# Kernel tuning notes

Hardware: AMD Instinct MI355X
Metric: run time of the kernel (lower is better)

Reference implementation:

```python
import jax, jax.numpy as jnp
import numpy as np

B, N, K = 2, 16384, 16
C_IN, C_OUT, SHARE = 64, 64, 8
ATTN = C_OUT // SHARE  # 8
EPS = 1e-5


def bn(x, gamma, beta):
    # BatchNorm2d_P: normalize over (B, N, K) per channel, training-mode batch stats
    m = jnp.mean(x, axis=(0, 1, 2), keepdims=True)
    v = jnp.var(x, axis=(0, 1, 2), keepdims=True)  # biased variance
    return (x - m) * jax.lax.rsqrt(v + EPS) * gamma + beta


def gather(points, idx):
    # points: (B, N, C), idx: (B, N, K) -> (B, N, K, C)
    b, n, k = idx.shape
    flat = idx.reshape(b, n * k)
    out = jnp.take_along_axis(points, flat[:, :, None], axis=1)
    return out.reshape(b, n, k, points.shape[-1])


def setup_inputs() -> dict:
    key = jax.random.key(0)
    ks = jax.random.split(key, 16)
    w = lambda k_, shp: (jax.random.normal(k_, shp, dtype=jnp.float32) * 0.02)
    inp = {
        "xyz": jax.random.normal(ks[0], (B, N, 3), dtype=jnp.float32),
        "features": jax.random.normal(ks[1], (B, N, C_IN), dtype=jnp.float32),
        "knn_idx": jax.random.randint(ks[2], (B, N, K), 0, N),
        "Wq": w(ks[3], (C_IN, C_OUT)), "bq": jnp.zeros((C_OUT,), jnp.float32),
        "Wk": w(ks[4], (C_IN, C_OUT)), "bk": jnp.zeros((C_OUT,), jnp.float32),
        "Wv": w(ks[5], (C_IN, C_OUT)), "bv": jnp.zeros((C_OUT,), jnp.float32),
        "Wd1": w(ks[6], (3, 3)), "bd1": jnp.zeros((3,), jnp.float32),
        "gamma_d": jnp.ones((3,), jnp.float32), "beta_d": jnp.zeros((3,), jnp.float32),
        "Wd2": w(ks[7], (3, C_OUT)), "bd2": jnp.zeros((C_OUT,), jnp.float32),
        "gamma_g1": jnp.ones((C_OUT,), jnp.float32), "beta_g1": jnp.zeros((C_OUT,), jnp.float32),
        "Wg1": w(ks[8], (C_OUT, ATTN)), "bg1": jnp.zeros((ATTN,), jnp.float32),
        "gamma_g2": jnp.ones((ATTN,), jnp.float32), "beta_g2": jnp.zeros((ATTN,), jnp.float32),
        "Wg2": w(ks[9], (ATTN, ATTN)), "bg2": jnp.zeros((ATTN,), jnp.float32),
    }
    return inp


def reference(xyz, features, knn_idx, Wq, bq, Wk, bk, Wv, bv,
              Wd1, bd1, gamma_d, beta_d, Wd2, bd2,
              gamma_g1, beta_g1, Wg1, bg1, gamma_g2, beta_g2, Wg2, bg2):
    q = features @ Wq + bq                       # (B,N,C_OUT)
    k = gather(features @ Wk + bk, knn_idx)      # (B,N,K,C_OUT)
    v = gather(features @ Wv + bv, knn_idx)      # (B,N,K,C_OUT)
    knn_xyz = gather(xyz, knn_idx)               # (B,N,K,3)
    rel = xyz[:, :, None, :] - knn_xyz           # (B,N,K,3)
    # fc_delta: Linear(3,3) -> BN -> ReLU -> Linear(3,C_OUT)
    pos_enc = jax.nn.relu(bn(rel @ Wd1 + bd1, gamma_d, beta_d)) @ Wd2 + bd2  # (B,N,K,C_OUT)
    # einops.reduce 'b n k (i j) -> b n k j' with j=mid_planes is identity (i=1)
    attn_in = q[:, :, None, :] - k + pos_enc     # (B,N,K,C_OUT)
    # fc_gamma: BN -> ReLU -> Linear(C_OUT,ATTN) -> BN -> ReLU -> Linear(ATTN,ATTN)
    h = jax.nn.relu(bn(attn_in, gamma_g1, beta_g1)) @ Wg1 + bg1  # (B,N,K,ATTN)
    h = jax.nn.relu(bn(h, gamma_g2, beta_g2)) @ Wg2 + bg2        # (B,N,K,ATTN)
    attn = jax.nn.softmax(h, axis=2)             # softmax over K neighbors
    vp = (v + pos_enc).reshape(B, N, K, SHARE, ATTN)
    res = jnp.einsum('bnksa,bnka->bnsa', vp, attn)
    return res.reshape(B, N, C_OUT)
```

## Files before the change

kernel.cpp:

```cpp
#include <hip/hip_runtime.h>
#include <hip/hip_bf16.h>

#define BB 2
#define NN 16384
#define KK 16
#define CC 64
#define AA 8
#define BN_PTS (BB*NN)
#define TOT (BB*NN*KK)
#define EPS 1e-5f

using bf = __hip_bfloat16;

__device__ __forceinline__ float ldf(const float* p, int i) { return p[i]; }
__device__ __forceinline__ float ldf(const bf* p, int i)    { return __bfloat162float(p[i]); }
__device__ __forceinline__ void  stf(float* p, int i, float v) { p[i] = v; }
__device__ __forceinline__ void  stf(bf* p, int i, float v)    { p[i] = __float2bfloat16(v); }

__device__ __forceinline__ float waveReduce(float v) {
    #pragma unroll
    for (int off = 32; off; off >>= 1) v += __shfl_down(v, off, 64);
    return v;
}

__global__ void detect_kernel(const unsigned* __restrict__ gbits, int* __restrict__ flag) {
    if (threadIdx.x == 0 && blockIdx.x == 0)
        *flag = (gbits[0] == 0x3F803F80u) ? 1 : 0;
}

template<typename T, int E>
__global__ __launch_bounds__(192) void qkv_kernel(
    const int* __restrict__ flag,
    const T* __restrict__ feat,
    const T* __restrict__ Wq, const T* __restrict__ bq,
    const T* __restrict__ Wk, const T* __restrict__ bk,
    const T* __restrict__ Wv, const T* __restrict__ bv,
    float* __restrict__ qf, float* __restrict__ kf, float* __restrict__ vf)
{
    if (*flag != E) return;
    __shared__ float fs[32*64];
    const int which = threadIdx.x / 64;
    const int c = threadIdx.x & 63;
    const T* W    = (which == 0) ? Wq : (which == 1) ? Wk : Wv;
    const T* bias = (which == 0) ? bq : (which == 1) ? bk : bv;
    float* out    = (which == 0) ? qf : (which == 1) ? kf : vf;

    float w[64];
    #pragma unroll
    for (int j = 0; j < 64; j++) w[j] = ldf(W, j*64 + c);
    const float bb_ = ldf(bias, c);

    const int row0 = blockIdx.x * 32;
    for (int i = threadIdx.x; i < 32*64; i += 192)
        fs[i] = ldf(feat, row0*64 + i);
    __syncthreads();

    for (int r = 0; r < 32; r++) {
        float acc = bb_;
        #pragma unroll
        for (int j = 0; j < 64; j++) acc = fmaf(fs[r*64 + j], w[j], acc);
        out[(row0 + r)*64 + c] = acc;
    }
}

template<typename T, int E>
__global__ __launch_bounds__(256) void statsd_kernel(
    const int* __restrict__ flag,
    const T* __restrict__ xyz, const int* __restrict__ knn,
    const T* __restrict__ Wd1, const T* __restrict__ bd1,
    float* __restrict__ part,
    float* __restrict__ dx, float* __restrict__ dy, float* __restrict__ dz)
{
    if (*flag != E) return;
    float w[9], bi[3];
    #pragma unroll
    for (int i = 0; i < 9; i++) w[i] = ldf(Wd1, i);
    #pragma unroll
    for (int i = 0; i < 3; i++) bi[i] = ldf(bd1, i);

    float s[6] = {0,0,0,0,0,0};
    const int tid = blockIdx.x * 256 + threadIdx.x;
    for (int p = tid; p < TOT; p += 256*256) {
        const int bn = p >> 4;
        const int b  = bn >> 14;
        const int j  = knn[p];
        const int nb = (b << 14) + j;
        const float r0 = ldf(xyz, bn*3+0) - ldf(xyz, nb*3+0);
        const float r1 = ldf(xyz, bn*3+1) - ldf(xyz, nb*3+1);
        const float r2 = ldf(xyz, bn*3+2) - ldf(xyz, nb*3+2);
        const float d0 = fmaf(r0, w[0], fmaf(r1, w[3], fmaf(r2, w[6], bi[0])));
        const float d1 = fmaf(r0, w[1], fmaf(r1, w[4], fmaf(r2, w[7], bi[1])));
        const float d2 = fmaf(r0, w[2], fmaf(r1, w[5], fmaf(r2, w[8], bi[2])));
        if (dx) { dx[p] = d0; dy[p] = d1; dz[p] = d2; }
        s[0] += d0; s[1] += d1; s[2] += d2;
        s[3] = fmaf(d0, d0, s[3]); s[4] = fmaf(d1, d1, s[4]); s[5] = fmaf(d2, d2, s[5]);
    }
    __shared__ float red[4*6];
    const int lane = threadIdx.x & 63, wave = threadIdx.x >> 6;
    #pragma unroll
    for (int i = 0; i < 6; i++) {
        const float r = waveReduce(s[i]);
        if (lane == 0) red[wave*6 + i] = r;
    }
    __syncthreads();
    if (threadIdx.x < 6)
        part[blockIdx.x*8 + threadIdx.x] =
            red[threadIdx.x] + red[6+threadIdx.x] + red[12+threadIdx.x] + red[18+threadIdx.x];
}

template<typename T, int E>
__global__ void finalize_d(const int* __restrict__ flag,
                           const float* __restrict__ part,
                           const T* __restrict__ gamma, const T* __restrict__ beta,
                           float* __restrict__ coef)
{
    if (*flag != E) return;
    __shared__ float sums[6];
    const int t = threadIdx.x;
    if (t < 6) {
        float s = 0;
        for (int b = 0; b < 256; b++) s += part[b*8 + t];
        sums[t] = s;
    }
    __syncthreads();
    if (t < 3) {
        const float mean = sums[t] / (float)TOT;
        const float var  = sums[3+t] / (float)TOT - mean*mean;
        const float sc   = ldf(gamma, t) * rsqrtf(var + EPS);
        coef[t]   = sc;
        coef[4+t] = ldf(beta, t) - mean*sc;
    }
}

template<typename T, int E>
__global__ __launch_bounds__(256) void statsg1_kernel(
    const int* __restrict__ flag,
    const T* __restrict__ xyz, const int* __restrict__ knn,
    const float* __restrict__ qf, const float* __restrict__ kf,
    const T* __restrict__ Wd1, const T* __restrict__ bd1,
    const T* __restrict__ Wd2, const T* __restrict__ bd2,
    const float* __restrict__ coefd, float* __restrict__ part,
    const float* __restrict__ dx, const float* __restrict__ dy,
    const float* __restrict__ dz, bf* __restrict__ aibuf)
{
    if (*flag != E) return;
    const int lane = threadIdx.x & 63, wave = threadIdx.x >> 6;
    float w1[9], b1[3], sc[3], sh[3];
    #pragma unroll
    for (int i = 0; i < 9; i++) w1[i] = ldf(Wd1, i);
    #pragma unroll
    for (int i = 0; i < 3; i++) { b1[i] = ldf(bd1, i); sc[i] = coefd[i]; sh[i] = coefd[4+i]; }
    const float w2a = ldf(Wd2, lane), w2b = ldf(Wd2, 64+lane), w2c = ldf(Wd2, 128+lane);
    const float bd2c = ldf(bd2, lane);

    float sum = 0.f, sq = 0.f;
    for (int bn = blockIdx.x*4 + wave; bn < BN_PTS; bn += 2048*4) {
        const int b = bn >> 14;
        const float qv = qf[bn*64 + lane];
        float x0 = 0.f, x1 = 0.f, x2 = 0.f;
        if (!dx) { x0 = ldf(xyz, bn*3+0); x1 = ldf(xyz, bn*3+1); x2 = ldf(xyz, bn*3+2); }
        #pragma unroll
        for (int k = 0; k < 16; k++) {
            const int it = bn*16 + k;
            const int j  = knn[it];
            const int nb = (b << 14) + j;
            float d0, d1, d2;
            if (dx) {
                d0 = dx[it]; d1 = dy[it]; d2 = dz[it];
            } else {
                const float r0 = x0 - ldf(xyz, nb*3+0);
                const float r1 = x1 - ldf(xyz, nb*3+1);
                const float r2 = x2 - ldf(xyz, nb*3+2);
                d0 = fmaf(r0, w1[0], fmaf(r1, w1[3], fmaf(r2, w1[6], b1[0])));
                d1 = fmaf(r0, w1[1], fmaf(r1, w1[4], fmaf(r2, w1[7], b1[1])));
                d2 = fmaf(r0, w1[2], fmaf(r1, w1[5], fmaf(r2, w1[8], b1[2])));
            }
            d0 = fmaxf(fmaf(d0, sc[0], sh[0]), 0.f);
            d1 = fmaxf(fmaf(d1, sc[1], sh[1]), 0.f);
            d2 = fmaxf(fmaf(d2, sc[2], sh[2]), 0.f);
            const float pos = fmaf(d0, w2a, fmaf(d1, w2b, fmaf(d2, w2c, bd2c)));
            const float at = qv - kf[nb*64 + lane] + pos;
            if (aibuf) aibuf[(size_t)it*64 + lane] = __float2bfloat16(at);
            sum += at; sq = fmaf(at, at, sq);
        }
    }
    __shared__ float ls[4][64], lq[4][64];
    ls[wave][lane] = sum; lq[wave][lane] = sq;
    __syncthreads();
    if (threadIdx.x < 64) {
        float a = 0.f, q = 0.f;
        #pragma unroll
        for (int w = 0; w < 4; w++) { a += ls[w][lane]; q += lq[w][lane]; }
        part[blockIdx.x*128 + lane]      = a;
        part[blockIdx.x*128 + 64 + lane] = q;
    }
}

template<int E>
__global__ __launch_bounds__(256) void reduce_g1(const int* __restrict__ flag,
                           const float* __restrict__ part, float* __restrict__ partB)
{
    if (*flag != E) return;
    __shared__ float red[2][128];
    const int t = threadIdx.x;
    const int col = t & 127, chunk = t >> 7;
    const int r0 = blockIdx.x * 32;
    float s = 0.f;
    #pragma unroll
    for (int j = 0; j < 16; j++) s += part[(r0 + chunk + 2*j)*128 + col];
    red[chunk][col] = s;
    __syncthreads();
    if (t < 128) partB[blockIdx.x*128 + t] = red[0][t] + red[1][t];
}

template<typename T, int E>
__global__ __launch_bounds__(512) void finalize_g1(const int* __restrict__ flag,
                            const float* __restrict__ partB,
                            const T* __restrict__ gamma, const T* __restrict__ beta,
                            float* __restrict__ coef)
{
    if (*flag != E) return;
    __shared__ float red[4][128];
    __shared__ float sums[128];
    const int t = threadIdx.x;
    const int col = t & 127, chunk = t >> 7;
    float s = 0.f;
    #pragma unroll
    for (int j = 0; j < 16; j++) s += partB[(chunk + 4*j)*128 + col];
    red[chunk][col] = s;
    __syncthreads();
    if (t < 128) sums[t] = red[0][t] + red[1][t] + red[2][t] + red[3][t];
    __syncthreads();
    if (t < 64) {
        const float mean = sums[t] / (float)TOT;
        const float var  = sums[64+t] / (float)TOT - mean*mean;
        const float sc   = ldf(gamma, t) * rsqrtf(var + EPS);
        coef[t]    = sc;
        coef[64+t] = ldf(beta, t) - mean*sc;
    }
}

template<typename T, int E>
__global__ __launch_bounds__(256) void h1_fast(
    const int* __restrict__ flag,
    const unsigned* __restrict__ aibuf,
    const float* __restrict__ coefg1,
    const T* __restrict__ Wg1, const T* __restrict__ bg1,
    float* __restrict__ h1, float* __restrict__ part)
{
    if (*flag != E) return;
    __shared__ float wg1s[512];
    __shared__ float scs[64], shs[64];
    __shared__ float ssum[4][8], ssq[4][8];
    const int t = threadIdx.x, lane = t & 63, wave = t >> 6;
    for (int i = t; i < 512; i += 256) wg1s[i] = ldf(Wg1, i);
    if (t < 64) { scs[t] = coefg1[t]; shs[t] = coefg1[64 + t]; }
    __syncthreads();

    const size_t item = (size_t)blockIdx.x*256 + t;
    const uint4* src = (const uint4*)aibuf + item*8;
    float h[8];
    #pragma unroll
    for (int a = 0; a < 8; a++) h[a] = ldf(bg1, a);
    #pragma unroll
    for (int cb = 0; cb < 8; cb++) {
        const uint4 u = src[cb];
        const unsigned uu[4] = {u.x, u.y, u.z, u.w};
        #pragma unroll
        for (int q = 0; q < 4; q++) {
            const int c0 = cb*8 + q*2;
            const float xlo = __uint_as_float(uu[q] << 16);
            const float xhi = __uint_as_float(uu[q] & 0xffff0000u);
            const float g0 = fmaxf(fmaf(xlo, scs[c0],   shs[c0]),   0.f);
            const float g1 = fmaxf(fmaf(xhi, scs[c0+1], shs[c0+1]), 0.f);
            #pragma unroll
            for (int a = 0; a < 8; a++) {
                h[a] = fmaf(g0, wg1s[c0*8 + a], h[a]);
                h[a] = fmaf(g1, wg1s[(c0+1)*8 + a], h[a]);
            }
        }
    }
    float4* hp = (float4*)(h1 + item*8);
    hp[0] = make_float4(h[0], h[1], h[2], h[3]);
    hp[1] = make_float4(h[4], h[5], h[6], h[7]);

    #pragma unroll
    for (int a = 0; a < 8; a++) {
        const float rs = waveReduce(h[a]);
        const float rq = waveReduce(h[a]*h[a]);
        if (lane == 0) { ssum[wave][a] = rs; ssq[wave][a] = rq; }
    }
    __syncthreads();
    if (t < 8) {
        part[blockIdx.x*16 + t]     = ssum[0][t] + ssum[1][t] + ssum[2][t] + ssum[3][t];
        part[blockIdx.x*16 + 8 + t] = ssq[0][t]  + ssq[1][t]  + ssq[2][t]  + ssq[3][t];
    }
}

#define H1_PAD 68
template<typename T, int E>
__global__ __launch_bounds__(256, 4) void h1_kernel(
    const int* __restrict__ flag,
    const T* __restrict__ xyz, const int* __restrict__ knn,
    const float* __restrict__ qf, const float* __restrict__ kf,
    const T* __restrict__ Wd1, const T* __restrict__ bd1,
    const T* __restrict__ Wd2, const T* __restrict__ bd2,
    const float* __restrict__ coefd, const float* __restrict__ coefg1,
    const T* __restrict__ Wg1, const T* __restrict__ bg1,
    float* __restrict__ h1, float* __restrict__ part)
{
    if (*flag != E) return;
    __shared__ float xs[128*H1_PAD];
    __shared__ float wg1s[512];
    __shared__ float ssum[4][8], ssq[4][8];
    const int t = threadIdx.x;
    const int lane = t & 63, wave = t >> 6;

    for (int i = t; i < 512; i += 256) wg1s[i] = ldf(Wg1, i);

    float w1[9], b1[3], scd[3], shd[3];
    #pragma unroll
    for (int i = 0; i < 9; i++) w1[i] = ldf(Wd1, i);
    #pragma unroll
    for (int i = 0; i < 3; i++) { b1[i] = ldf(bd1, i); scd[i] = coefd[i]; shd[i] = coefd[4+i]; }
    const float w2a = ldf(Wd2, lane), w2b = ldf(Wd2, 64+lane), w2c = ldf(Wd2, 128+lane);
    const float bd2c = ldf(bd2, lane);
    const float sc1 = coefg1[lane], sh1 = coefg1[64+lane];
    const int lslot = (lane < 32) ? lane : lane + 4;

    #pragma unroll
    for (int g = 0; g < 2; g++) {
        const int pl = wave*2 + g;
        const int bn = blockIdx.x*8 + pl;
        const int b  = bn >> 14;
        const float qv = qf[bn*64 + lane];
        const float x0 = ldf(xyz, bn*3+0), x1 = ldf(xyz, bn*3+1), x2 = ldf(xyz, bn*3+2);
        #pragma unroll
        for (int k = 0; k < 16; k++) {
            const int j  = knn[bn*16 + k];
            const int nb = (b << 14) + j;
            const float r0 = x0 - ldf(xyz, nb*3+0);
            const float r1 = x1 - ldf(xyz, nb*3+1);
            const float r2 = x2 - ldf(xyz, nb*3+2);
            float d0 = fmaf(r0, w1[0], fmaf(r1, w1[3], fmaf(r2, w1[6], b1[0])));
            float d1 = fmaf(r0, w1[1], fmaf(r1, w1[4], fmaf(r2, w1[7], b1[1])));
            float d2 = fmaf(r0, w1[2], fmaf(r1, w1[5], fmaf(r2, w1[8], b1[2])));
            d0 = fmaxf(fmaf(d0, scd[0], shd[0]), 0.f);
            d1 = fmaxf(fmaf(d1, scd[1], shd[1]), 0.f);
            d2 = fmaxf(fmaf(d2, scd[2], shd[2]), 0.f);
            const float pos = fmaf(d0, w2a, fmaf(d1, w2b, fmaf(d2, w2c, bd2c)));
            const float at = qv - kf[nb*64 + lane] + pos;
            xs[(pl*16 + k)*H1_PAD + lslot] = fmaxf(fmaf(at, sc1, sh1), 0.f);
        }
    }
    __syncthreads();

    const int item = t >> 1;
    const int half = t & 1;
    float h[8];
    #pragma unroll
    for (int a = 0; a < 8; a++) h[a] = half ? 0.f : ldf(bg1, a);
    const float4* xr = (const float4*)(xs + item*H1_PAD + half*36);
    const float* wbase = wg1s + half*256;
    #pragma unroll
    for (int cb = 0; cb < 8; cb++) {
        const float4 xv = xr[cb];
        #pragma unroll
        for (int jj = 0; jj < 4; jj++) {
            const float x = (jj == 0) ? xv.x : (jj == 1) ? xv.y : (jj == 2) ? xv.z : xv.w;
            const float4 wa = *(const float4*)&wbase[(cb*4 + jj)*8];
            const float4 wb = *(const float4*)&wbase[(cb*4 + jj)*8 + 4];
            h[0] = fmaf(x, wa.x, h[0]); h[1] = fmaf(x, wa.y, h[1]);
            h[2] = fmaf(x, wa.z, h[2]); h[3] = fmaf(x, wa.w, h[3]);
            h[4] = fmaf(x, wb.x, h[4]); h[5] = fmaf(x, wb.y, h[5]);
            h[6] = fmaf(x, wb.z, h[6]); h[7] = fmaf(x, wb.w, h[7]);
        }
    }
    #pragma unroll
    for (int a = 0; a < 8; a++) h[a] += __shfl_xor(h[a], 1, 64);

    const int it = blockIdx.x*128 + item;
    if (half == 0) {
        float4* hp = (float4*)(h1 + (size_t)it*8);
        hp[0] = make_float4(h[0], h[1], h[2], h[3]);
        hp[1] = make_float4(h[4], h[5], h[6], h[7]);
    }

    #pragma unroll
    for (int a = 0; a < 8; a++) {
        const float rs = waveReduce(h[a]);
        const float rq = waveReduce(h[a]*h[a]);
        if (lane == 0) { ssum[wave][a] = 0.5f*rs; ssq[wave][a] = 0.5f*rq; }
    }
    __syncthreads();
    if (t < 8) {
        part[blockIdx.x*16 + t]     = ssum[0][t] + ssum[1][t] + ssum[2][t] + ssum[3][t];
        part[blockIdx.x*16 + 8 + t] = ssq[0][t]  + ssq[1][t]  + ssq[2][t]  + ssq[3][t];
    }
}

template<int E>
__global__ __launch_bounds__(256) void reduce_g2(const int* __restrict__ flag,
                           const float* __restrict__ part, float* __restrict__ partB,
                           int rows)
{
    if (*flag != E) return;
    __shared__ float red[16][16];
    const int t = threadIdx.x;
    const int col = t & 15, chunk = t >> 4;
    const int rpb = rows >> 6;
    const int r0 = blockIdx.x * rpb;
    float s = 0.f;
    for (int r = chunk; r < rpb; r += 16) s += part[(r0 + r)*16 + col];
    red[chunk][col] = s;
    __syncthreads();
    if (t < 16) {
        float a = 0.f;
        #pragma unroll
        for (int c = 0; c < 16; c++) a += red[c][t];
        partB[blockIdx.x*16 + t] = a;
    }
}

template<typename T, int E>
__global__ __launch_bounds__(256) void finalize_g2(const int* __restrict__ flag,
                            const float* __restrict__ partB,
                            const T* __restrict__ gamma, const T* __restrict__ beta,
                            float* __restrict__ coef)
{
    if (*flag != E) return;
    __shared__ float red[16][16];
    __shared__ float sums[16];
    const int t = threadIdx.x;
    const int col = t & 15, chunk = t >> 4;
    float s = 0.f;
    #pragma unroll
    for (int j = 0; j < 4; j++) s += partB[(chunk + 16*j)*16 + col];
    red[chunk][col] = s;
    __syncthreads();
    if (t < 16) {
        float a = 0.f;
        #pragma unroll
        for (int c = 0; c < 16; c++) a += red[c][t];
        sums[t] = a;
    }
    __syncthreads();
    if (t < 8) {
        const float mean = sums[t] / (float)TOT;
        const float var  = sums[8+t] / (float)TOT - mean*mean;
        const float sc   = ldf(gamma, t) * rsqrtf(var + EPS);
        coef[t]   = sc;
        coef[8+t] = ldf(beta, t) - mean*sc;
    }
}

template<typename T, int E>
__global__ __launch_bounds__(256) void out_kernel(
    const int* __restrict__ flag,
    const T* __restrict__ xyz, const int* __restrict__ knn,
    const float* __restrict__ vf, const float* __restrict__ h1,
    const T* __restrict__ Wd1, const T* __restrict__ bd1,
    const T* __restrict__ Wd2, const T* __restrict__ bd2,
    const float* __restrict__ coefd, const float* __restrict__ coefg2,
    const T* __restrict__ Wg2, const T* __restrict__ bg2,
    const float* __restrict__ dx, const float* __restrict__ dy,
    const float* __restrict__ dz,
    T* __restrict__ out)
{
    if (*flag != E) return;
    __shared__ float g[4][128];
    __shared__ float hh[4][128];
    __shared__ float dd[4][16][3];
    __shared__ int   idxs[4][16];
    __shared__ float wg2[64];
    const int t = threadIdx.x;
    const int bn0 = blockIdx.x * 4;

    if (t < 64) wg2[t] = ldf(Wg2, t);

    {
        const int p = t >> 6, f = t & 63;
        const int base = (bn0 + p) * 128;
        #pragma unroll
        for (int i = 0; i < 2; i++) {
            const int ff = f + i*64;
            const int a = ff & 7;
            const float v = h1[base + ff];
            g[p][ff] = fmaxf(fmaf(v, coefg2[a], coefg2[8 + a]), 0.f);
        }
    }
    if (t < 64) {
        const int p = t >> 4, k = t & 15;
        const int bn = bn0 + p;
        const int b = bn >> 14;
        const int it = bn*16 + k;
        const int j = knn[it];
        idxs[p][k] = j;
        float d0, d1, d2;
        if (dx) {
            d0 = dx[it]; d1 = dy[it]; d2 = dz[it];
        } else {
            const int nb = (b << 14) + j;
            const float r0 = ldf(xyz, bn*3+0) - ldf(xyz, nb*3+0);
            const float r1 = ldf(xyz, bn*3+1) - ldf(xyz, nb*3+1);
            const float r2 = ldf(xyz, bn*3+2) - ldf(xyz, nb*3+2);
            d0 = fmaf(r0, ldf(Wd1,0), fmaf(r1, ldf(Wd1,3), fmaf(r2, ldf(Wd1,6), ldf(bd1,0))));
            d1 = fmaf(r0, ldf(Wd1,1), fmaf(r1, ldf(Wd1,4), fmaf(r2, ldf(Wd1,7), ldf(bd1,1))));
            d2 = fmaf(r0, ldf(Wd1,2), fmaf(r1, ldf(Wd1,5), fmaf(r2, ldf(Wd1,8), ldf(bd1,2))));
        }
        dd[p][k][0] = fmaxf(fmaf(d0, coefd[0], coefd[4]), 0.f);
        dd[p][k][1] = fmaxf(fmaf(d1, coefd[1], coefd[5]), 0.f);
        dd[p][k][2] = fmaxf(fmaf(d2, coefd[2], coefd[6]), 0.f);
    }
    __syncthreads();

    {
        #pragma unroll
        for (int i = 0; i < 2; i++) {
            const int o = t + i*256;
            const int p = o >> 7, f = o & 127;
            const int a = f & 7, k = f >> 3;
            float acc = ldf(bg2, a);
            #pragma unroll
            for (int jj = 0; jj < 8; jj++) acc = fmaf(g[p][k*8 + jj], wg2[jj*8 + a], acc);
            hh[p][f] = acc;
        }
    }
    __syncthreads();

    if (t < 32) {
        const int p = t >> 3, a = t & 7;
        float m = -1e30f;
        #pragma unroll
        for (int k = 0; k < 16; k++) m = fmaxf(m, hh[p][k*8 + a]);
        float e[16]; float s = 0.f;
        #pragma unroll
        for (int k = 0; k < 16; k++) { e[k] = __expf(hh[p][k*8 + a] - m); s += e[k]; }
        const float inv = 1.f / s;
        #pragma unroll
        for (int k = 0; k < 16; k++) hh[p][k*8 + a] = e[k] * inv;
    }
    __syncthreads();

    {
        const int p = t >> 6, c = t & 63, a = c & 7;
        const int bn = bn0 + p;
        const int b = bn >> 14;
        const float w0 = ldf(Wd2, c), w1 = ldf(Wd2, 64 + c), w2 = ldf(Wd2, 128 + c);
        const float bd2c = ldf(bd2, c);
        float acc = 0.f;
        #pragma unroll
        for (int k = 0; k < 16; k++) {
            const int j = idxs[p][k];
            const float pos = fmaf(dd[p][k][0], w0, fmaf(dd[p][k][1], w1, fmaf(dd[p][k][2], w2, bd2c)));
            const float vv = vf[((b << 14) + j)*64 + c] + pos;
            acc = fmaf(vv, hh[p][k*8 + a], acc);
        }
        stf(out, bn*64 + c, acc);
    }
}

#define WS_BIG_FLOATS 29108384ull

template<typename T, int E>
static void launch_all(void* const* d_in, void* d_out, float* ws, const int* flag,
                       bool big, hipStream_t stream) {
    const T*   xyz   = (const T*) d_in[0];
    const T*   feat  = (const T*) d_in[1];
    const int* knn   = (const int*)d_in[2];
    const T*   Wq    = (const T*) d_in[3];
    const T*   bq    = (const T*) d_in[4];
    const T*   Wk    = (const T*) d_in[5];
    const T*   bk    = (const T*) d_in[6];
    const T*   Wv    = (const T*) d_in[7];
    const T*   bv    = (const T*) d_in[8];
    const T*   Wd1   = (const T*) d_in[9];
    const T*   bd1   = (const T*) d_in[10];
    const T*   gd    = (const T*) d_in[11];
    const T*   betad = (const T*) d_in[12];
    const T*   Wd2   = (const T*) d_in[13];
    const T*   bd2   = (const T*) d_in[14];
    const T*   gg1   = (const T*) d_in[15];
    const T*   bg1b  = (const T*) d_in[16];
    const T*   Wg1   = (const T*) d_in[17];
    const T*   bg1   = (const T*) d_in[18];
    const T*   gg2   = (const T*) d_in[19];
    const T*   bg2b  = (const T*) d_in[20];
    const T*   Wg2   = (const T*) d_in[21];
    const T*   bg2   = (const T*) d_in[22];
    T* out = (T*)d_out;

    float* qf      = ws;
    float* kf      = ws + 2097152;
    float* vf      = ws + 4194304;
    float* h1      = ws + 6291456;
    float* part_d  = ws + 10485760;
    float* partA   = ws + 10487808;
    float* partB   = ws + 10749952;
    float* coef_d  = ws + 10758144;
    float* coef_g1 = ws + 10758152;
    float* coef_g2 = ws + 10758280;
    float* dx      = big ? ws + 10758304 : nullptr;
    float* dy      = big ? ws + 11282592 : nullptr;
    float* dz      = big ? ws + 11806880 : nullptr;
    bf*    aibuf   = big ? (bf*)(ws + 12331168) : nullptr;

    qkv_kernel<T,E><<<1024, 192, 0, stream>>>(flag, feat, Wq, bq, Wk, bk, Wv, bv, qf, kf, vf);
    statsd_kernel<T,E><<<256, 256, 0, stream>>>(flag, xyz, knn, Wd1, bd1, part_d, dx, dy, dz);
    finalize_d<T,E><<<1, 64, 0, stream>>>(flag, part_d, gd, betad, coef_d);
    statsg1_kernel<T,E><<<2048, 256, 0, stream>>>(flag, xyz, knn, qf, kf, Wd1, bd1, Wd2, bd2,
                                                  coef_d, partA, dx, dy, dz, aibuf);
    reduce_g1<E><<<64, 256, 0, stream>>>(flag, partA, partB);
    finalize_g1<T,E><<<1, 512, 0, stream>>>(flag, partB, gg1, bg1b, coef_g1);
    if (big) {
        h1_fast<T,E><<<2048, 256, 0, stream>>>(flag, (const unsigned*)aibuf, coef_g1,
                                               Wg1, bg1, h1, partA);
        reduce_g2<E><<<64, 256, 0, stream>>>(flag, partA, partB, 2048);
    } else {
        h1_kernel<T,E><<<4096, 256, 0, stream>>>(flag, xyz, knn, qf, kf, Wd1, bd1, Wd2, bd2,
                                                 coef_d, coef_g1, Wg1, bg1, h1, partA);
        reduce_g2<E><<<64, 256, 0, stream>>>(flag, partA, partB, 4096);
    }
    finalize_g2<T,E><<<1, 256, 0, stream>>>(flag, partB, gg2, bg2b, coef_g2);
    out_kernel<T,E><<<8192, 256, 0, stream>>>(flag, xyz, knn, vf, h1, Wd1, bd1, Wd2, bd2,
                                              coef_d, coef_g2, Wg2, bg2, dx, dy, dz, out);
}

extern "C" void kernel_launch(void* const* d_in, const int* in_sizes, int n_in,
                              void* d_out, int out_size, void* d_ws, size_t ws_size,
                              hipStream_t stream) {
    float* ws = (float*)d_ws;
    int* flag = (int*)(ws + 10758296);
    const bool big = ws_size >= WS_BIG_FLOATS * 4ull;

    detect_kernel<<<1, 1, 0, stream>>>((const unsigned*)d_in[11], flag);

    launch_all<float, 0>(d_in, d_out, ws, flag, big, stream);
    launch_all<bf,    1>(d_in, d_out, ws, flag, big, stream);
}
```

Before: 277.6 us.

## Merge dtype-specialized launches into single kernels and store K projection in bf16

Each stage used to be launched twice, once per input dtype, with the inactive copy returning early on a device flag. Now each kernel is launched once and branches on the flag inside the kernel to a templated body, using dynamic shared memory. This roughly halves the number of kernel launches. The K projection buffer is also stored in bf16, which halves the bytes moved by the random neighbor gather in statsg1 (and in h1_kernel on the fallback path). The trade-off is extra rounding error in k.

After: 270.7 us. 2.5% less time.

```diff
diff --git a/kernel.cpp b/kernel.cpp
--- a/kernel.cpp
+++ b/kernel.cpp
@@ -1,5 +1,6 @@
 #include <hip/hip_runtime.h>
 #include <hip/hip_bf16.h>
+#include <type_traits>
 
 #define BB 2
 #define NN 16384
@@ -12,10 +13,16 @@
 
 using bf = __hip_bfloat16;
 
-__device__ __forceinline__ float ldf(const float* p, int i) { return p[i]; }
-__device__ __forceinline__ float ldf(const bf* p, int i)    { return __bfloat162float(p[i]); }
-__device__ __forceinline__ void  stf(float* p, int i, float v) { p[i] = v; }
-__device__ __forceinline__ void  stf(bf* p, int i, float v)    { p[i] = __float2bfloat16(v); }
+__device__ __forceinline__ float b2f(bf x) { return __bfloat162float(x); }
+
+template<typename T> __device__ __forceinline__ float ldt(const void* p, int i) {
+    if constexpr (std::is_same<T, bf>::value) return b2f(((const bf*)p)[i]);
+    else return ((const float*)p)[i];
+}
+template<typename T> __device__ __forceinline__ void stt(void* p, int i, float v) {
+    if constexpr (std::is_same<T, bf>::value) ((bf*)p)[i] = __float2bfloat16(v);
+    else ((float*)p)[i] = v;
+}
 
 __device__ __forceinline__ float waveReduce(float v) {
     #pragma unroll
@@ -28,55 +35,57 @@
         *flag = (gbits[0] == 0x3F803F80u) ? 1 : 0;
 }
 
-template<typename T, int E>
+template<typename T>
+__device__ void qkv_body(float* smem,
+    const void* feat, const void* Wq, const void* bq, const void* Wk, const void* bk,
+    const void* Wv, const void* bv, float* qf, bf* kfb, float* vf)
+{
+    float* fs = smem;
+    const int which = threadIdx.x / 64;
+    const int c = threadIdx.x & 63;
+    const void* W    = (which == 0) ? Wq : (which == 1) ? Wk : Wv;
+    const void* bias = (which == 0) ? bq : (which == 1) ? bk : bv;
+
+    float w[64];
+    #pragma unroll
+    for (int j = 0; j < 64; j++) w[j] = ldt<T>(W, j*64 + c);
+    const float bb_ = ldt<T>(bias, c);
+
+    const int row0 = blockIdx.x * 32;
+    for (int i = threadIdx.x; i < 32*64; i += 192)
+        fs[i] = ldt<T>(feat, row0*64 + i);
+    __syncthreads();
+
+    for (int r = 0; r < 32; r++) {
+        float acc = bb_;
+        #pragma unroll
+        for (int j = 0; j < 64; j++) acc = fmaf(fs[r*64 + j], w[j], acc);
+        const int idx = (row0 + r)*64 + c;
+        if (which == 1)      kfb[idx] = __float2bfloat16(acc);
+        else if (which == 0) qf[idx] = acc;
+        else                 vf[idx] = acc;
+    }
+}
 __global__ __launch_bounds__(192) void qkv_kernel(
     const int* __restrict__ flag,
-    const T* __restrict__ feat,
-    const T* __restrict__ Wq, const T* __restrict__ bq,
-    const T* __restrict__ Wk, const T* __restrict__ bk,
-    const T* __restrict__ Wv, const T* __restrict__ bv,
-    float* __restrict__ qf, float* __restrict__ kf, float* __restrict__ vf)
-{
-    if (*flag != E) return;
-    __shared__ float fs[32*64];
-    const int which = threadIdx.x / 64;
-    const int c = threadIdx.x & 63;
-    const T* W    = (which == 0) ? Wq : (which == 1) ? Wk : Wv;
-    const T* bias = (which == 0) ? bq : (which == 1) ? bk : bv;
-    float* out    = (which == 0) ? qf : (which == 1) ? kf : vf;
-
-    float w[64];
-    #pragma unroll
-    for (int j = 0; j < 64; j++) w[j] = ldf(W, j*64 + c);
-    const float bb_ = ldf(bias, c);
-
-    const int row0 = blockIdx.x * 32;
-    for (int i = threadIdx.x; i < 32*64; i += 192)
-        fs[i] = ldf(feat, row0*64 + i);
-    __syncthreads();
-
-    for (int r = 0; r < 32; r++) {
-        float acc = bb_;
-        #pragma unroll
-        for (int j = 0; j < 64; j++) acc = fmaf(fs[r*64 + j], w[j], acc);
-        out[(row0 + r)*64 + c] = acc;
-    }
-}
-
-template<typename T, int E>
-__global__ __launch_bounds__(256) void statsd_kernel(
-    const int* __restrict__ flag,
-    const T* __restrict__ xyz, const int* __restrict__ knn,
-    const T* __restrict__ Wd1, const T* __restrict__ bd1,
-    float* __restrict__ part,
-    float* __restrict__ dx, float* __restrict__ dy, float* __restrict__ dz)
-{
-    if (*flag != E) return;
+    const void* feat, const void* Wq, const void* bq, const void* Wk, const void* bk,
+    const void* Wv, const void* bv, float* qf, bf* kfb, float* vf)
+{
+    extern __shared__ float smem[];
+    if (*flag) qkv_body<bf>(smem, feat, Wq, bq, Wk, bk, Wv, bv, qf, kfb, vf);
+    else       qkv_body<float>(smem, feat, Wq, bq, Wk, bk, Wv, bv, qf, kfb, vf);
+}
+
+template<typename T>
+__device__ void statsd_body(float* smem,
+    const void* xyz, const int* knn, const void* Wd1, const void* bd1,
+    float* part, float* dx, float* dy, float* dz)
+{
     float w[9], bi[3];
     #pragma unroll
-    for (int i = 0; i < 9; i++) w[i] = ldf(Wd1, i);
-    #pragma unroll
-    for (int i = 0; i < 3; i++) bi[i] = ldf(bd1, i);
+    for (int i = 0; i < 9; i++) w[i] = ldt<T>(Wd1, i);
+    #pragma unroll
+    for (int i = 0; i < 3; i++) bi[i] = ldt<T>(bd1, i);
 
     float s[6] = {0,0,0,0,0,0};
     const int tid = blockIdx.x * 256 + threadIdx.x;
@@ -85,9 +94,9 @@
         const int b  = bn >> 14;
         const int j  = knn[p];
         const int nb = (b << 14) + j;
-        const float r0 = ldf(xyz, bn*3+0) - ldf(xyz, nb*3+0);
-        const float r1 = ldf(xyz, bn*3+1) - ldf(xyz, nb*3+1);
-        const float r2 = ldf(xyz, bn*3+2) - ldf(xyz, nb*3+2);
+        const float r0 = ldt<T>(xyz, bn*3+0) - ldt<T>(xyz, nb*3+0);
+        const float r1 = ldt<T>(xyz, bn*3+1) - ldt<T>(xyz, nb*3+1);
+        const float r2 = ldt<T>(xyz, bn*3+2) - ldt<T>(xyz, nb*3+2);
         const float d0 = fmaf(r0, w[0], fmaf(r1, w[3], fmaf(r2, w[6], bi[0])));
         const float d1 = fmaf(r0, w[1], fmaf(r1, w[4], fmaf(r2, w[7], bi[1])));
         const float d2 = fmaf(r0, w[2], fmaf(r1, w[5], fmaf(r2, w[8], bi[2])));
@@ -95,7 +104,7 @@
         s[0] += d0; s[1] += d1; s[2] += d2;
         s[3] = fmaf(d0, d0, s[3]); s[4] = fmaf(d1, d1, s[4]); s[5] = fmaf(d2, d2, s[5]);
     }
-    __shared__ float red[4*6];
+    float* red = smem;
     const int lane = threadIdx.x & 63, wave = threadIdx.x >> 6;
     #pragma unroll
     for (int i = 0; i < 6; i++) {
@@ -107,15 +116,20 @@
         part[blockIdx.x*8 + threadIdx.x] =
             red[threadIdx.x] + red[6+threadIdx.x] + red[12+threadIdx.x] + red[18+threadIdx.x];
 }
-
-template<typename T, int E>
-__global__ void finalize_d(const int* __restrict__ flag,
-                           const float* __restrict__ part,
-                           const T* __restrict__ gamma, const T* __restrict__ beta,
-                           float* __restrict__ coef)
-{
-    if (*flag != E) return;
-    __shared__ float sums[6];
+__global__ __launch_bounds__(256) void statsd_kernel(
+    const int* __restrict__ flag,
+    const void* xyz, const int* __restrict__ knn, const void* Wd1, const void* bd1,
+    float* part, float* dx, float* dy, float* dz)
+{
+    extern __shared__ float smem[];
+    if (*flag) statsd_body<bf>(smem, xyz, knn, Wd1, bd1, part, dx, dy, dz);
+    else       statsd_body<float>(smem, xyz, knn, Wd1, bd1, part, dx, dy, dz);
+}
+
+template<typename T>
+__device__ void finalize_d_body(float* sums,
+    const float* part, const void* gamma, const void* beta, float* coef)
+{
     const int t = threadIdx.x;
     if (t < 6) {
         float s = 0;
@@ -126,39 +140,41 @@
     if (t < 3) {
         const float mean = sums[t] / (float)TOT;
         const float var  = sums[3+t] / (float)TOT - mean*mean;
-        const float sc   = ldf(gamma, t) * rsqrtf(var + EPS);
+        const float sc   = ldt<T>(gamma, t) * rsqrtf(var + EPS);
         coef[t]   = sc;
-        coef[4+t] = ldf(beta, t) - mean*sc;
-    }
-}
-
-template<typename T, int E>
-__global__ __launch_bounds__(256) void statsg1_kernel(
-    const int* __restrict__ flag,
-    const T* __restrict__ xyz, const int* __restrict__ knn,
-    const float* __restrict__ qf, const float* __restrict__ kf,
-    const T* __restrict__ Wd1, const T* __restrict__ bd1,
-    const T* __restrict__ Wd2, const T* __restrict__ bd2,
-    const float* __restrict__ coefd, float* __restrict__ part,
-    const float* __restrict__ dx, const float* __restrict__ dy,
-    const float* __restrict__ dz, bf* __restrict__ aibuf)
-{
-    if (*flag != E) return;
+        coef[4+t] = ldt<T>(beta, t) - mean*sc;
+    }
+}
+__global__ void finalize_d(const int* __restrict__ flag, const float* __restrict__ part,
+                           const void* gamma, const void* beta, float* coef)
+{
+    extern __shared__ float smem[];
+    if (*flag) finalize_d_body<bf>(smem, part, gamma, beta, coef);
+    else       finalize_d_body<float>(smem, part, gamma, beta, coef);
+}
+
+template<typename T>
+__device__ void statsg1_body(float* smem,
+    const void* xyz, const int* knn, const float* qf, const bf* kfb,
+    const void* Wd1, const void* bd1, const void* Wd2, const void* bd2,
+    const float* coefd, float* part,
+    const float* dx, const float* dy, const float* dz, bf* aibuf)
+{
     const int lane = threadIdx.x & 63, wave = threadIdx.x >> 6;
     float w1[9], b1[3], sc[3], sh[3];
     #pragma unroll
-    for (int i = 0; i < 9; i++) w1[i] = ldf(Wd1, i);
-    #pragma unroll
-    for (int i = 0; i < 3; i++) { b1[i] = ldf(bd1, i); sc[i] = coefd[i]; sh[i] = coefd[4+i]; }
-    const float w2a = ldf(Wd2, lane), w2b = ldf(Wd2, 64+lane), w2c = ldf(Wd2, 128+lane);
-    const float bd2c = ldf(bd2, lane);
+    for (int i = 0; i < 9; i++) w1[i] = ldt<T>(Wd1, i);
+    #pragma unroll
+    for (int i = 0; i < 3; i++) { b1[i] = ldt<T>(bd1, i); sc[i] = coefd[i]; sh[i] = coefd[4+i]; }
+    const float w2a = ldt<T>(Wd2, lane), w2b = ldt<T>(Wd2, 64+lane), w2c = ldt<T>(Wd2, 128+lane);
+    const float bd2c = ldt<T>(bd2, lane);
 
     float sum = 0.f, sq = 0.f;
     for (int bn = blockIdx.x*4 + wave; bn < BN_PTS; bn += 2048*4) {
         const int b = bn >> 14;
         const float qv = qf[bn*64 + lane];
         float x0 = 0.f, x1 = 0.f, x2 = 0.f;
-        if (!dx) { x0 = ldf(xyz, bn*3+0); x1 = ldf(xyz, bn*3+1); x2 = ldf(xyz, bn*3+2); }
+        if (!dx) { x0 = ldt<T>(xyz, bn*3+0); x1 = ldt<T>(xyz, bn*3+1); x2 = ldt<T>(xyz, bn*3+2); }
         #pragma unroll
         for (int k = 0; k < 16; k++) {
             const int it = bn*16 + k;
@@ -168,9 +184,9 @@
             if (dx) {
                 d0 = dx[it]; d1 = dy[it]; d2 = dz[it];
             } else {
-                const float r0 = x0 - ldf(xyz, nb*3+0);
-                const float r1 = x1 - ldf(xyz, nb*3+1);
-                const float r2 = x2 - ldf(xyz, nb*3+2);
+                const float r0 = x0 - ldt<T>(xyz, nb*3+0);
+                const float r1 = x1 - ldt<T>(xyz, nb*3+1);
+                const float r2 = x2 - ldt<T>(xyz, nb*3+2);
                 d0 = fmaf(r0, w1[0], fmaf(r1, w1[3], fmaf(r2, w1[6], b1[0])));
                 d1 = fmaf(r0, w1[1], fmaf(r1, w1[4], fmaf(r2, w1[7], b1[1])));
                 d2 = fmaf(r0, w1[2], fmaf(r1, w1[5], fmaf(r2, w1[8], b1[2])));
@@ -179,28 +195,39 @@
             d1 = fmaxf(fmaf(d1, sc[1], sh[1]), 0.f);
             d2 = fmaxf(fmaf(d2, sc[2], sh[2]), 0.f);
             const float pos = fmaf(d0, w2a, fmaf(d1, w2b, fmaf(d2, w2c, bd2c)));
-            const float at = qv - kf[nb*64 + lane] + pos;
+            const float at = qv - b2f(kfb[nb*64 + lane]) + pos;
             if (aibuf) aibuf[(size_t)it*64 + lane] = __float2bfloat16(at);
             sum += at; sq = fmaf(at, at, sq);
         }
     }
-    __shared__ float ls[4][64], lq[4][64];
-    ls[wave][lane] = sum; lq[wave][lane] = sq;
+    float* ls = smem;
+    float* lq = smem + 256;
+    ls[wave*64 + lane] = sum; lq[wave*64 + lane] = sq;
     __syncthreads();
     if (threadIdx.x < 64) {
         float a = 0.f, q = 0.f;
         #pragma unroll
-        for (int w = 0; w < 4; w++) { a += ls[w][lane]; q += lq[w][lane]; }
+        for (int w = 0; w < 4; w++) { a += ls[w*64 + lane]; q += lq[w*64 + lane]; }
         part[blockIdx.x*128 + lane]      = a;
         part[blockIdx.x*128 + 64 + lane] = q;
     }
 }
-
-template<int E>
-__global__ __launch_bounds__(256) void reduce_g1(const int* __restrict__ flag,
-                           const float* __restrict__ part, float* __restrict__ partB)
-{
-    if (*flag != E) return;
+__global__ __launch_bounds__(256) void statsg1_kernel(
+    const int* __restrict__ flag,
+    const void* xyz, const int* __restrict__ knn, const float* __restrict__ qf,
+    const bf* __restrict__ kfb,
+    const void* Wd1, const void* bd1, const void* Wd2, const void* bd2,
+    const float* __restrict__ coefd, float* part,
+    const float* dx, const float* dy, const float* dz, bf* aibuf)
+{
+    extern __shared__ float smem[];
+    if (*flag) statsg1_body<bf>(smem, xyz, knn, qf, kfb, Wd1, bd1, Wd2, bd2, coefd, part, dx, dy, dz, aibuf);
+    else       statsg1_body<float>(smem, xyz, knn, qf, kfb, Wd1, bd1, Wd2, bd2, coefd, part, dx, dy, dz, aibuf);
+}
+
+__global__ __launch_bounds__(256) void reduce_g1(const float* __restrict__ part,
+                                                 float* __restrict__ partB)
+{
     __shared__ float red[2][128];
     const int t = threadIdx.x;
     const int col = t & 127, chunk = t >> 7;
@@ -213,47 +240,49 @@
     if (t < 128) partB[blockIdx.x*128 + t] = red[0][t] + red[1][t];
 }
 
-template<typename T, int E>
-__global__ __launch_bounds__(512) void finalize_g1(const int* __restrict__ flag,
-                            const float* __restrict__ partB,
-                            const T* __restrict__ gamma, const T* __restrict__ beta,
-                            float* __restrict__ coef)
-{
-    if (*flag != E) return;
-    __shared__ float red[4][128];
-    __shared__ float sums[128];
+template<typename T>
+__device__ void finalize_g1_body(float* smem,
+    const float* partB, const void* gamma, const void* beta, float* coef)
+{
+    float* red  = smem;
+    float* sums = smem + 512;
     const int t = threadIdx.x;
     const int col = t & 127, chunk = t >> 7;
     float s = 0.f;
     #pragma unroll
     for (int j = 0; j < 16; j++) s += partB[(chunk + 4*j)*128 + col];
-    red[chunk][col] = s;
-    __syncthreads();
-    if (t < 128) sums[t] = red[0][t] + red[1][t] + red[2][t] + red[3][t];
+    red[chunk*128 + col] = s;
+    __syncthreads();
+    if (t < 128) sums[t] = red[t] + red[128+t] + red[256+t] + red[384+t];
     __syncthreads();
     if (t < 64) {
         const float mean = sums[t] / (float)TOT;
         const float var  = sums[64+t] / (float)TOT - mean*mean;
-        const float sc   = ldf(gamma, t) * rsqrtf(var + EPS);
+        const float sc   = ldt<T>(gamma, t) * rsqrtf(var + EPS);
         coef[t]    = sc;
-        coef[64+t] = ldf(beta, t) - mean*sc;
-    }
-}
-
-template<typename T, int E>
-__global__ __launch_bounds__(256) void h1_fast(
-    const int* __restrict__ flag,
-    const unsigned* __restrict__ aibuf,
-    const float* __restrict__ coefg1,
-    const T* __restrict__ Wg1, const T* __restrict__ bg1,
-    float* __restrict__ h1, float* __restrict__ part)
-{
-    if (*flag != E) return;
-    __shared__ float wg1s[512];
-    __shared__ float scs[64], shs[64];
-    __shared__ float ssum[4][8], ssq[4][8];
+        coef[64+t] = ldt<T>(beta, t) - mean*sc;
+    }
+}
+__global__ __launch_bounds__(512) void finalize_g1(const int* __restrict__ flag,
+    const float* __restrict__ partB, const void* gamma, const void* beta, float* coef)
+{
+    extern __shared__ float smem[];
+    if (*flag) finalize_g1_body<bf>(smem, partB, gamma, beta, coef);
+    else       finalize_g1_body<float>(smem, partB, gamma, beta, coef);
+}
+
+template<typename T>
+__device__ void h1_fast_body(float* smem,
+    const unsigned* aibuf, const float* coefg1, const void* Wg1, const void* bg1,
+    float* h1, float* part)
+{
+    float* wg1s = smem;
+    float* scs  = smem + 512;
+    float* shs  = smem + 576;
+    float* ssum = smem + 640;
+    float* ssq  = smem + 672;
     const int t = threadIdx.x, lane = t & 63, wave = t >> 6;
-    for (int i = t; i < 512; i += 256) wg1s[i] = ldf(Wg1, i);
+    for (int i = t; i < 512; i += 256) wg1s[i] = ldt<T>(Wg1, i);
     if (t < 64) { scs[t] = coefg1[t]; shs[t] = coefg1[64 + t]; }
     __syncthreads();
 
@@ -261,7 +290,7 @@
     const uint4* src = (const uint4*)aibuf + item*8;
     float h[8];
     #pragma unroll
-    for (int a = 0; a < 8; a++) h[a] = ldf(bg1, a);
+    for (int a = 0; a < 8; a++) h[a] = ldt<T>(bg1, a);
     #pragma unroll
     for (int cb = 0; cb < 8; cb++) {
         const uint4 u = src[cb];
@@ -288,43 +317,47 @@
     for (int a = 0; a < 8; a++) {
         const float rs = waveReduce(h[a]);
         const float rq = waveReduce(h[a]*h[a]);
-        if (lane == 0) { ssum[wave][a] = rs; ssq[wave][a] = rq; }
+        if (lane == 0) { ssum[wave*8 + a] = rs; ssq[wave*8 + a] = rq; }
     }
     __syncthreads();
     if (t < 8) {
-        part[blockIdx.x*16 + t]     = ssum[0][t] + ssum[1][t] + ssum[2][t] + ssum[3][t];
-        part[blockIdx.x*16 + 8 + t] = ssq[0][t]  + ssq[1][t]  + ssq[2][t]  + ssq[3][t];
-    }
+        part[blockIdx.x*16 + t]     = ssum[t] + ssum[8+t] + ssum[16+t] + ssum[24+t];
+        part[blockIdx.x*16 + 8 + t] = ssq[t]  + ssq[8+t]  + ssq[16+t]  + ssq[24+t];
+    }
+}
+__global__ __launch_bounds__(256) void h1_fast(const int* __restrict__ flag,
+    const unsigned* __restrict__ aibuf, const float* __restrict__ coefg1,
+    const void* Wg1, const void* bg1, float* h1, float* part)
+{
+    extern __shared__ float smem[];
+    if (*flag) h1_fast_body<bf>(smem, aibuf, coefg1, Wg1, bg1, h1, part);
+    else       h1_fast_body<float>(smem, aibuf, coefg1, Wg1, bg1, h1, part);
 }
 
 #define H1_PAD 68
-template<typename T, int E>
-__global__ __launch_bounds__(256, 4) void h1_kernel(
-    const int* __restrict__ flag,
-    const T* __restrict__ xyz, const int* __restrict__ knn,
-    const float* __restrict__ qf, const float* __restrict__ kf,
-    const T* __restrict__ Wd1, const T* __restrict__ bd1,
-    const T* __restrict__ Wd2, const T* __restrict__ bd2,
-    const float* __restrict__ coefd, const float* __restrict__ coefg1,
-    const T* __restrict__ Wg1, const T* __restrict__ bg1,
-    float* __restrict__ h1, float* __restrict__ part)
-{
-    if (*flag != E) return;
-    __shared__ float xs[128*H1_PAD];
-    __shared__ float wg1s[512];
-    __shared__ float ssum[4][8], ssq[4][8];
+template<typename T>
+__device__ void h1_body(float* smem,
+    const void* xyz, const int* knn, const float* qf, const bf* kfb,
+    const void* Wd1, const void* bd1, const void* Wd2, const void* bd2,
+    const float* coefd, const float* coefg1, const void* Wg1, const void* bg1,
+    float* h1, float* part)
+{
+    float* xs   = smem;
+    float* wg1s = smem + 8704;
+    float* ssum = smem + 9216;
+    float* ssq  = smem + 9248;
     const int t = threadIdx.x;
     const int lane = t & 63, wave = t >> 6;
 
-    for (int i = t; i < 512; i += 256) wg1s[i] = ldf(Wg1, i);
+    for (int i = t; i < 512; i += 256) wg1s[i] = ldt<T>(Wg1, i);
 
     float w1[9], b1[3], scd[3], shd[3];
     #pragma unroll
-    for (int i = 0; i < 9; i++) w1[i] = ldf(Wd1, i);
-    #pragma unroll
-    for (int i = 0; i < 3; i++) { b1[i] = ldf(bd1, i); scd[i] = coefd[i]; shd[i] = coefd[4+i]; }
-    const float w2a = ldf(Wd2, lane), w2b = ldf(Wd2, 64+lane), w2c = ldf(Wd2, 128+lane);
-    const float bd2c = ldf(bd2, lane);
+    for (int i = 0; i < 9; i++) w1[i] = ldt<T>(Wd1, i);
+    #pragma unroll
+    for (int i = 0; i < 3; i++) { b1[i] = ldt<T>(bd1, i); scd[i] = coefd[i]; shd[i] = coefd[4+i]; }
+    const float w2a = ldt<T>(Wd2, lane), w2b = ldt<T>(Wd2, 64+lane), w2c = ldt<T>(Wd2, 128+lane);
+    const float bd2c = ldt<T>(bd2, lane);
     const float sc1 = coefg1[lane], sh1 = coefg1[64+lane];
     const int lslot = (lane < 32) ? lane : lane + 4;
 
@@ -334,14 +367,14 @@
         const int bn = blockIdx.x*8 + pl;
         const int b  = bn >> 14;
         const float qv = qf[bn*64 + lane];
-        const float x0 = ldf(xyz, bn*3+0), x1 = ldf(xyz, bn*3+1), x2 = ldf(xyz, bn*3+2);
+        const float x0 = ldt<T>(xyz, bn*3+0), x1 = ldt<T>(xyz, bn*3+1), x2 = ldt<T>(xyz, bn*3+2);
         #pragma unroll
         for (int k = 0; k < 16; k++) {
             const int j  = knn[bn*16 + k];
             const int nb = (b << 14) + j;
-            const float r0 = x0 - ldf(xyz, nb*3+0);
-            const float r1 = x1 - ldf(xyz, nb*3+1);
-            const float r2 = x2 - ldf(xyz, nb*3+2);
+            const float r0 = x0 - ldt<T>(xyz, nb*3+0);
+            const float r1 = x1 - ldt<T>(xyz, nb*3+1);
+            const float r2 = x2 - ldt<T>(xyz, nb*3+2);
             float d0 = fmaf(r0, w1[0], fmaf(r1, w1[3], fmaf(r2, w1[6], b1[0])));
             float d1 = fmaf(r0, w1[1], fmaf(r1, w1[4], fmaf(r2, w1[7], b1[1])));
             float d2 = fmaf(r0, w1[2], fmaf(r1, w1[5], fmaf(r2, w1[8], b1[2])));
@@ -349,7 +382,7 @@
             d1 = fmaxf(fmaf(d1, scd[1], shd[1]), 0.f);
             d2 = fmaxf(fmaf(d2, scd[2], shd[2]), 0.f);
             const float pos = fmaf(d0, w2a, fmaf(d1, w2b, fmaf(d2, w2c, bd2c)));
-            const float at = qv - kf[nb*64 + lane] + pos;
+            const float at = qv - b2f(kfb[nb*64 + lane]) + pos;
             xs[(pl*16 + k)*H1_PAD + lslot] = fmaxf(fmaf(at, sc1, sh1), 0.f);
         }
     }
@@ -359,7 +392,7 @@
     const int half = t & 1;
     float h[8];
     #pragma unroll
-    for (int a = 0; a < 8; a++) h[a] = half ? 0.f : ldf(bg1, a);
+    for (int a = 0; a < 8; a++) h[a] = half ? 0.f : ldt<T>(bg1, a);
     const float4* xr = (const float4*)(xs + item*H1_PAD + half*36);
     const float* wbase = wg1s + half*256;
     #pragma unroll
@@ -385,26 +418,33 @@
         hp[0] = make_float4(h[0], h[1], h[2], h[3]);
         hp[1] = make_float4(h[4], h[5], h[6], h[7]);
     }
-
     #pragma unroll
     for (int a = 0; a < 8; a++) {
         const float rs = waveReduce(h[a]);
         const float rq = waveReduce(h[a]*h[a]);
-        if (lane == 0) { ssum[wave][a] = 0.5f*rs; ssq[wave][a] = 0.5f*rq; }
+        if (lane == 0) { ssum[wave*8 + a] = 0.5f*rs; ssq[wave*8 + a] = 0.5f*rq; }
     }
     __syncthreads();
     if (t < 8) {
-        part[blockIdx.x*16 + t]     = ssum[0][t] + ssum[1][t] + ssum[2][t] + ssum[3][t];
-        part[blockIdx.x*16 + 8 + t] = ssq[0][t]  + ssq[1][t]  + ssq[2][t]  + ssq[3][t];
-    }
-}
-
-template<int E>
-__global__ __launch_bounds__(256) void reduce_g2(const int* __restrict__ flag,
-                           const float* __restrict__ part, float* __restrict__ partB,
-                           int rows)
-{
-    if (*flag != E) return;
+        part[blockIdx.x*16 + t]     = ssum[t] + ssum[8+t] + ssum[16+t] + ssum[24+t];
+        part[blockIdx.x*16 + 8 + t] = ssq[t]  + ssq[8+t]  + ssq[16+t]  + ssq[24+t];
+    }
+}
+__global__ __launch_bounds__(256, 4) void h1_kernel(const int* __restrict__ flag,
+    const void* xyz, const int* __restrict__ knn, const float* __restrict__ qf,
+    const bf* __restrict__ kfb,
+    const void* Wd1, const void* bd1, const void* Wd2, const void* bd2,
+    const float* __restrict__ coefd, const float* __restrict__ coefg1,
+    const void* Wg1, const void* bg1, float* h1, float* part)
+{
+    extern __shared__ float smem[];
+    if (*flag) h1_body<bf>(smem, xyz, knn, qf, kfb, Wd1, bd1, Wd2, bd2, coefd, coefg1, Wg1, bg1, h1, part);
+    else       h1_body<float>(smem, xyz, knn, qf, kfb, Wd1, bd1, Wd2, bd2, coefd, coefg1, Wg1, bg1, h1, part);
+}
+
+__global__ __launch_bounds__(256) void reduce_g2(const float* __restrict__ part,
+                                                 float* __restrict__ partB, int rows)
+{
     __shared__ float red[16][16];
     const int t = threadIdx.x;
     const int col = t & 15, chunk = t >> 4;
@@ -422,61 +462,58 @@
     }
 }
 
-template<typename T, int E>
-__global__ __launch_bounds__(256) void finalize_g2(const int* __restrict__ flag,
-                            const float* __restrict__ partB,
-                            const T* __restrict__ gamma, const T* __restrict__ beta,
-                            float* __restrict__ coef)
-{
-    if (*flag != E) return;
-    __shared__ float red[16][16];
-    __shared__ float sums[16];
+template<typename T>
+__device__ void finalize_g2_body(float* smem,
+    const float* partB, const void* gamma, const void* beta, float* coef)
+{
+    float* red  = smem;
+    float* sums = smem + 256;
     const int t = threadIdx.x;
     const int col = t & 15, chunk = t >> 4;
     float s = 0.f;
     #pragma unroll
     for (int j = 0; j < 4; j++) s += partB[(chunk + 16*j)*16 + col];
-    red[chunk][col] = s;
+    red[chunk*16 + col] = s;
     __syncthreads();
     if (t < 16) {
         float a = 0.f;
         #pragma unroll
-        for (int c = 0; c < 16; c++) a += red[c][t];
+        for (int c = 0; c < 16; c++) a += red[c*16 + t];
         sums[t] = a;
     }
     __syncthreads();
     if (t < 8) {
         const float mean = sums[t] / (float)TOT;
         const float var  = sums[8+t] / (float)TOT - mean*mean;
-        const float sc   = ldf(gamma, t) * rsqrtf(var + EPS);
+        const float sc   = ldt<T>(gamma, t) * rsqrtf(var + EPS);
         coef[t]   = sc;
-        coef[8+t] = ldf(beta, t) - mean*sc;
-    }
-}
-
-template<typename T, int E>
-__global__ __launch_bounds__(256) void out_kernel(
-    const int* __restrict__ flag,
-    const T* __restrict__ xyz, const int* __restrict__ knn,
-    const float* __restrict__ vf, const float* __restrict__ h1,
-    const T* __restrict__ Wd1, const T* __restrict__ bd1,
-    const T* __restrict__ Wd2, const T* __restrict__ bd2,
-    const float* __restrict__ coefd, const float* __restrict__ coefg2,
-    const T* __restrict__ Wg2, const T* __restrict__ bg2,
-    const float* __restrict__ dx, const float* __restrict__ dy,
-    const float* __restrict__ dz,
-    T* __restrict__ out)
-{
-    if (*flag != E) return;
-    __shared__ float g[4][128];
-    __shared__ float hh[4][128];
-    __shared__ float dd[4][16][3];
-    __shared__ int   idxs[4][16];
-    __shared__ float wg2[64];
+        coef[8+t] = ldt<T>(beta, t) - mean*sc;
+    }
+}
+__global__ __launch_bounds__(256) void finalize_g2(const int* __restrict__ flag,
+    const float* __restrict__ partB, const void* gamma, const void* beta, float* coef)
+{
+    extern __shared__ float smem[];
+    if (*flag) finalize_g2_body<bf>(smem, partB, gamma, beta, coef);
+    else       finalize_g2_body<float>(smem, partB, gamma, beta, coef);
+}
+
+template<typename T>
+__device__ void out_body(float* smem,
+    const void* xyz, const int* knn, const float* vf, const float* h1,
+    const void* Wd1, const void* bd1, const void* Wd2, const void* bd2,
+    const float* coefd, const float* coefg2, const void* Wg2, const void* bg2,
+    const float* dx, const float* dy, const float* dz, void* out)
+{
+    float* g   = smem;
+    float* hh  = smem + 512;
+    float* dd  = smem + 1024;
+    float* wg2 = smem + 1216;
+    int*  idxs = (int*)(smem + 1280);
     const int t = threadIdx.x;
     const int bn0 = blockIdx.x * 4;
 
-    if (t < 64) wg2[t] = ldf(Wg2, t);
+    if (t < 64) wg2[t] = ldt<T>(Wg2, t);
 
     {
         const int p = t >> 6, f = t & 63;
@@ -486,7 +523,7 @@
             const int ff = f + i*64;
             const int a = ff & 7;
             const float v = h1[base + ff];
-            g[p][ff] = fmaxf(fmaf(v, coefg2[a], coefg2[8 + a]), 0.f);
+            g[p*128 + ff] = fmaxf(fmaf(v, coefg2[a], coefg2[8 + a]), 0.f);
         }
     }
     if (t < 64) {
@@ -495,22 +532,22 @@
         const int b = bn >> 14;
         const int it = bn*16 + k;
         const int j = knn[it];
-        idxs[p][k] = j;
+        idxs[p*16 + k] = j;
         float d0, d1, d2;
         if (dx) {
             d0 = dx[it]; d1 = dy[it]; d2 = dz[it];
         } else {
             const int nb = (b << 14) + j;
-            const float r0 = ldf(xyz, bn*3+0) - ldf(xyz, nb*3+0);
-            const float r1 = ldf(xyz, bn*3+1) - ldf(xyz, nb*3+1);
-            const float r2 = ldf(xyz, bn*3+2) - ldf(xyz, nb*3+2);
-            d0 = fmaf(r0, ldf(Wd1,0), fmaf(r1, ldf(Wd1,3), fmaf(r2, ldf(Wd1,6), ldf(bd1,0))));
-            d1 = fmaf(r0, ldf(Wd1,1), fmaf(r1, ldf(Wd1,4), fmaf(r2, ldf(Wd1,7), ldf(bd1,1))));
-            d2 = fmaf(r0, ldf(Wd1,2), fmaf(r1, ldf(Wd1,5), fmaf(r2, ldf(Wd1,8), ldf(bd1,2))));
-        }
-        dd[p][k][0] = fmaxf(fmaf(d0, coefd[0], coefd[4]), 0.f);
-        dd[p][k][1] = fmaxf(fmaf(d1, coefd[1], coefd[5]), 0.f);
-        dd[p][k][2] = fmaxf(fmaf(d2, coefd[2], coefd[6]), 0.f);
+            const float r0 = ldt<T>(xyz, bn*3+0) - ldt<T>(xyz, nb*3+0);
+            const float r1 = ldt<T>(xyz, bn*3+1) - ldt<T>(xyz, nb*3+1);
+            const float r2 = ldt<T>(xyz, bn*3+2) - ldt<T>(xyz, nb*3+2);
+            d0 = fmaf(r0, ldt<T>(Wd1,0), fmaf(r1, ldt<T>(Wd1,3), fmaf(r2, ldt<T>(Wd1,6), ldt<T>(bd1,0))));
+            d1 = fmaf(r0, ldt<T>(Wd1,1), fmaf(r1, ldt<T>(Wd1,4), fmaf(r2, ldt<T>(Wd1,7), ldt<T>(bd1,1))));
+            d2 = fmaf(r0, ldt<T>(Wd1,2), fmaf(r1, ldt<T>(Wd1,5), fmaf(r2, ldt<T>(Wd1,8), ldt<T>(bd1,2))));
+        }
+        dd[(p*16 + k)*3 + 0] = fmaxf(fmaf(d0, coefd[0], coefd[4]), 0.f);
+        dd[(p*16 + k)*3 + 1] = fmaxf(fmaf(d1, coefd[1], coefd[5]), 0.f);
+        dd[(p*16 + k)*3 + 2] = fmaxf(fmaf(d2, coefd[2], coefd[6]), 0.f);
     }
     __syncthreads();
 
@@ -520,10 +557,10 @@
             const int o = t + i*256;
             const int p = o >> 7, f = o & 127;
             const int a = f & 7, k = f >> 3;
-            float acc = ldf(bg2, a);
+            float acc = ldt<T>(bg2, a);
             #pragma unroll
-            for (int jj = 0; jj < 8; jj++) acc = fmaf(g[p][k*8 + jj], wg2[jj*8 + a], acc);
-            hh[p][f] = acc;
+            for (int jj = 0; jj < 8; jj++) acc = fmaf(g[p*128 + k*8 + jj], wg2[jj*8 + a], acc);
+            hh[p*128 + f] = acc;
         }
     }
     __syncthreads();
@@ -532,13 +569,13 @@
         const int p = t >> 3, a = t & 7;
         float m = -1e30f;
         #pragma unroll
-        for (int k = 0; k < 16; k++) m = fmaxf(m, hh[p][k*8 + a]);
+        for (int k = 0; k < 16; k++) m = fmaxf(m, hh[p*128 + k*8 + a]);
         float e[16]; float s = 0.f;
         #pragma unroll
-        for (int k = 0; k < 16; k++) { e[k] = __expf(hh[p][k*8 + a] - m); s += e[k]; }
+        for (int k = 0; k < 16; k++) { e[k] = __expf(hh[p*128 + k*8 + a] - m); s += e[k]; }
         const float inv = 1.f / s;
         #pragma unroll
-        for (int k = 0; k < 16; k++) hh[p][k*8 + a] = e[k] * inv;
+        for (int k = 0; k < 16; k++) hh[p*128 + k*8 + a] = e[k] * inv;
     }
     __syncthreads();
 
@@ -546,95 +583,83 @@
         const int p = t >> 6, c = t & 63, a = c & 7;
         const int bn = bn0 + p;
         const int b = bn >> 14;
-        const float w0 = ldf(Wd2, c), w1 = ldf(Wd2, 64 + c), w2 = ldf(Wd2, 128 + c);
-        const float bd2c = ldf(bd2, c);
+        const float w0 = ldt<T>(Wd2, c), w1 = ldt<T>(Wd2, 64 + c), w2 = ldt<T>(Wd2, 128 + c);
+        const float bd2c = ldt<T>(bd2, c);
         float acc = 0.f;
         #pragma unroll
         for (int k = 0; k < 16; k++) {
-            const int j = idxs[p][k];
-            const float pos = fmaf(dd[p][k][0], w0, fmaf(dd[p][k][1], w1, fmaf(dd[p][k][2], w2, bd2c)));
+            const int j = idxs[p*16 + k];
+            const float pos = fmaf(dd[(p*16+k)*3+0], w0, fmaf(dd[(p*16+k)*3+1], w1,
+                              fmaf(dd[(p*16+k)*3+2], w2, bd2c)));
             const float vv = vf[((b << 14) + j)*64 + c] + pos;
-            acc = fmaf(vv, hh[p][k*8 + a], acc);
-        }
-        stf(out, bn*64 + c, acc);
-    }
-}
-
-#define WS_BIG_FLOATS 29108384ull
-
-template<typename T, int E>
-static void launch_all(void* const* d_in, void* d_out, float* ws, const int* flag,
-                       bool big, hipStream_t stream) {
-    const T*   xyz   = (const T*) d_in[0];
-    const T*   feat  = (const T*) d_in[1];
-    const int* knn   = (const int*)d_in[2];
-    const T*   Wq    = (const T*) d_in[3];
-    const T*   bq    = (const T*) d_in[4];
-    const T*   Wk    = (const T*) d_in[5];
-    const T*   bk    = (const T*) d_in[6];
-    const T*   Wv    = (const T*) d_in[7];
-    const T*   bv    = (const T*) d_in[8];
-    const T*   Wd1   = (const T*) d_in[9];
-    const T*   bd1   = (const T*) d_in[10];
-    const T*   gd    = (const T*) d_in[11];
-    const T*   betad = (const T*) d_in[12];
-    const T*   Wd2   = (const T*) d_in[13];
-    const T*   bd2   = (const T*) d_in[14];
-    const T*   gg1   = (const T*) d_in[15];
-    const T*   bg1b  = (const T*) d_in[16];
-    const T*   Wg1   = (const T*) d_in[17];
-    const T*   bg1   = (const T*) d_in[18];
-    const T*   gg2   = (const T*) d_in[19];
-    const T*   bg2b  = (const T*) d_in[20];
-    const T*   Wg2   = (const T*) d_in[21];
-    const T*   bg2   = (const T*) d_in[22];
-    T* out = (T*)d_out;
-
-    float* qf      = ws;
-    float* kf      = ws + 2097152;
-    float* vf      = ws + 4194304;
-    float* h1      = ws + 6291456;
-    float* part_d  = ws + 10485760;
-    float* partA   = ws + 10487808;
-    float* partB   = ws + 10749952;
-    float* coef_d  = ws + 10758144;
-    float* coef_g1 = ws + 10758152;
-    float* coef_g2 = ws + 10758280;
-    float* dx      = big ? ws + 10758304 : nullptr;
-    float* dy      = big ? ws + 11282592 : nullptr;
-    float* dz      = big ? ws + 11806880 : nullptr;
-    bf*    aibuf   = big ? (bf*)(ws + 12331168) : nullptr;
-
-    qkv_kernel<T,E><<<1024, 192, 0, stream>>>(flag, feat, Wq, bq, Wk, bk, Wv, bv, qf, kf, vf);
-    statsd_kernel<T,E><<<256, 256, 0, stream>>>(flag, xyz, knn, Wd1, bd1, part_d, dx, dy, dz);
-    finalize_d<T,E><<<1, 64, 0, stream>>>(flag, part_d, gd, betad, coef_d);
-    statsg1_kernel<T,E><<<2048, 256, 0, stream>>>(flag, xyz, knn, qf, kf, Wd1, bd1, Wd2, bd2,
-                                                  coef_d, partA, dx, dy, dz, aibuf);
-    reduce_g1<E><<<64, 256, 0, stream>>>(flag, partA, partB);
-    finalize_g1<T,E><<<1, 512, 0, stream>>>(flag, partB, gg1, bg1b, coef_g1);
-    if (big) {
-        h1_fast<T,E><<<2048, 256, 0, stream>>>(flag, (const unsigned*)aibuf, coef_g1,
-                                               Wg1, bg1, h1, partA);
-        reduce_g2<E><<<64, 256, 0, stream>>>(flag, partA, partB, 2048);
-    } else {
-        h1_kernel<T,E><<<4096, 256, 0, stream>>>(flag, xyz, knn, qf, kf, Wd1, bd1, Wd2, bd2,
-                                                 coef_d, coef_g1, Wg1, bg1, h1, partA);
-        reduce_g2<E><<<64, 256, 0, stream>>>(flag, partA, partB, 4096);
-    }
-    finalize_g2<T,E><<<1, 256, 0, stream>>>(flag, partB, gg2, bg2b, coef_g2);
-    out_kernel<T,E><<<8192, 256, 0, stream>>>(flag, xyz, knn, vf, h1, Wd1, bd1, Wd2, bd2,
-                                              coef_d, coef_g2, Wg2, bg2, dx, dy, dz, out);
-}
+            acc = fmaf(vv, hh[p*128 + k*8 + a], acc);
+        }
+        stt<T>(out, bn*64 + c, acc);
+    }
+}
+__global__ __launch_bounds__(256) void out_kernel(const int* __restrict__ flag,
+    const void* xyz, const int* __restrict__ knn, const float* __restrict__ vf,
+    const float* __restrict__ h1,
+    const void* Wd1, const void* bd1, const void* Wd2, const void* bd2,
+    const float* __restrict__ coefd, const float* __restrict__ coefg2,
+    const void* Wg2, const void* bg2,
+    const float* dx, const float* dy, const float* dz, void* out)
+{
+    extern __shared__ float smem[];
+    if (*flag) out_body<bf>(smem, xyz, knn, vf, h1, Wd1, bd1, Wd2, bd2, coefd, coefg2, Wg2, bg2, dx, dy, dz, out);
+    else       out_body<float>(smem, xyz, knn, vf, h1, Wd1, bd1, Wd2, bd2, coefd, coefg2, Wg2, bg2, dx, dy, dz, out);
+}
+
+#define WS_BIG_FLOATS 28059808ull
 
 extern "C" void kernel_launch(void* const* d_in, const int* in_sizes, int n_in,
                               void* d_out, int out_size, void* d_ws, size_t ws_size,
                               hipStream_t stream) {
     float* ws = (float*)d_ws;
-    int* flag = (int*)(ws + 10758296);
+    const void* xyz  = d_in[0];
+    const void* feat = d_in[1];
+    const int*  knn  = (const int*)d_in[2];
+    const void *Wq = d_in[3], *bq = d_in[4], *Wk = d_in[5], *bk = d_in[6];
+    const void *Wv = d_in[7], *bv = d_in[8], *Wd1 = d_in[9], *bd1 = d_in[10];
+    const void *gd = d_in[11], *betad = d_in[12], *Wd2 = d_in[13], *bd2 = d_in[14];
+    const void *gg1 = d_in[15], *bg1b = d_in[16], *Wg1 = d_in[17], *bg1 = d_in[18];
+    const void *gg2 = d_in[19], *bg2b = d_in[20], *Wg2 = d_in[21], *bg2 = d_in[22];
+
+    float* qf      = ws;
+    bf*    kfb     = (bf*)(ws + 2097152);
+    float* vf      = ws + 3145728;
+    float* h1      = ws + 5242880;
+    float* part_d  = ws + 9437184;
+    float* partA   = ws + 9439232;
+    float* partB   = ws + 9701376;
+    float* coef_d  = ws + 9709568;
+    float* coef_g1 = ws + 9709576;
+    float* coef_g2 = ws + 9709704;
+    int*   flag    = (int*)(ws + 9709720);
     const bool big = ws_size >= WS_BIG_FLOATS * 4ull;
+    float* dx      = big ? ws + 9709728  : nullptr;
+    float* dy      = big ? ws + 10234016 : nullptr;
+    float* dz      = big ? ws + 10758304 : nullptr;
+    bf*    aibuf   = big ? (bf*)(ws + 11282592) : nullptr;
 
     detect_kernel<<<1, 1, 0, stream>>>((const unsigned*)d_in[11], flag);
-
-    launch_all<float, 0>(d_in, d_out, ws, flag, big, stream);
-    launch_all<bf,    1>(d_in, d_out, ws, flag, big, stream);
-}
+    qkv_kernel<<<1024, 192, 8192, stream>>>(flag, feat, Wq, bq, Wk, bk, Wv, bv, qf, kfb, vf);
+    statsd_kernel<<<256, 256, 128, stream>>>(flag, xyz, knn, Wd1, bd1, part_d, dx, dy, dz);
+    finalize_d<<<1, 64, 32, stream>>>(flag, part_d, gd, betad, coef_d);
+    statsg1_kernel<<<2048, 256, 2048, stream>>>(flag, xyz, knn, qf, kfb, Wd1, bd1, Wd2, bd2,
+                                                coef_d, partA, dx, dy, dz, aibuf);
+    reduce_g1<<<64, 256, 0, stream>>>(partA, partB);
+    finalize_g1<<<1, 512, 2560, stream>>>(flag, partB, gg1, bg1b, coef_g1);
+    if (big) {
+        h1_fast<<<2048, 256, 2816, stream>>>(flag, (const unsigned*)aibuf, coef_g1,
+                                             Wg1, bg1, h1, partA);
+        reduce_g2<<<64, 256, 0, stream>>>(partA, partB, 2048);
+    } else {
+        h1_kernel<<<4096, 256, 37120, stream>>>(flag, xyz, knn, qf, kfb, Wd1, bd1, Wd2, bd2,
+                                                coef_d, coef_g1, Wg1, bg1, h1, partA);
+        reduce_g2<<<64, 256, 0, stream>>>(partA, partB, 4096);
+    }
+    finalize_g2<<<1, 256, 1088, stream>>>(flag, partB, gg2, bg2b, coef_g2);
+    out_kernel<<<8192, 256, 5376, stream>>>(flag, xyz, knn, vf, h1, Wd1, bd1, Wd2, bd2,
+                                            coef_d, coef_g2, Wg2, bg2, dx, dy, dz, d_out);
+}
```
